# Optimization experiments

Measured on AMD Instinct MI355X. Metric: run time of the kernel, lower is better.

Reference implementation:

```python
import jax, jax.numpy as jnp
import numpy as np

EPS = 1e-12  # matches torch.nn.functional.normalize default eps


def _l2norm(x, axis=-1):
    # F.normalize: x / max(||x||, eps)
    n = jnp.sqrt(jnp.sum(x * x, axis=axis, keepdims=True))
    return x / jnp.maximum(n, EPS)


def setup_inputs() -> dict:
    key = jax.random.key(0)
    k1, k2, k3 = jax.random.split(key, 3)
    batch, n_mels, time_steps = 32, 80, 4000
    num_codebooks, codebook_size, d = 2, 1024, 64
    mel = jax.random.normal(k1, (batch, n_mels, time_steps), dtype=jnp.float32)
    proj = jax.random.normal(k2, (num_codebooks, n_mels, d), dtype=jnp.float32)
    codebooks = jax.random.normal(k3, (num_codebooks, codebook_size, d), dtype=jnp.float32)
    return {"mel": mel, "proj": proj, "codebooks": codebooks}


def reference(mel, proj, codebooks):
    # mel: [b, n, t] -> [b, t, n]
    mel_t = jnp.transpose(mel, (0, 2, 1))
    # project for all codebooks at once: [c, b, t, d]
    p = jnp.einsum('btn,cnd->cbtd', mel_t, proj)
    p = _l2norm(p, axis=-1)
    cb = _l2norm(codebooks, axis=-1)  # [c, k, d]
    # cosine similarity: [c, b, t, k]
    sim = jnp.einsum('cbtd,ckd->cbtk', p, cb)
    codes = jnp.argmax(sim, axis=-1)  # [c, b, t]
    return codes
```

## Files before the change

kernel.cpp:

```cpp
#include <hip/hip_runtime.h>
#include <hip/hip_bf16.h>
#include <math.h>
#include <stdint.h>


#define B      32
#define NMELS  80
#define TSTEPS 4000
#define NCB    2
#define KCB    1024
#define DDIM   64
#define TPB    256
#define TM     64
#define KT     64
#define NKT    (KCB / KT)
#define PPAD   66

typedef short bf16x8 __attribute__((ext_vector_type(8)));
typedef float f32x4  __attribute__((ext_vector_type(4)));

#define WS_CB_OFF   8192
#define WS_NEEDED   (8192 + NCB*KCB*DDIM*2)

static __device__ __forceinline__ uint32_t bits(float f) {
    return __builtin_bit_cast(uint32_t, f);
}
static __device__ __forceinline__ float fbits(uint32_t u) {
    return __builtin_bit_cast(float, u);
}
static __device__ __forceinline__ uint32_t rne16(uint32_t u) {
    return (u + 0x7FFFu + ((u >> 16) & 1u)) >> 16;
}

__global__ __launch_bounds__(TPB) void rpq_prep(const float* __restrict__ cb,
                                                float* __restrict__ ws)
{
    const int idx = blockIdx.x * TPB + threadIdx.x;
    if (idx >= NCB * KCB) return;

    const float4* row = (const float4*)(cb + (size_t)idx * DDIM);
    float4 v[16];
    float ss = 0.f;
    #pragma unroll
    for (int i = 0; i < 16; ++i) {
        v[i] = row[i];
        ss += v[i].x*v[i].x + v[i].y*v[i].y + v[i].z*v[i].z + v[i].w*v[i].w;
    }
    const float inv = 1.0f / fmaxf(sqrtf(ss), 1e-12f);
    ws[idx] = inv;

    uint32_t dw[32];
    #pragma unroll
    for (int i = 0; i < 16; ++i) {
        dw[2*i]   = rne16(bits(v[i].x * inv)) | (rne16(bits(v[i].y * inv)) << 16);
        dw[2*i+1] = rne16(bits(v[i].z * inv)) | (rne16(bits(v[i].w * inv)) << 16);
    }
    uint4* dst = (uint4*)((char*)ws + WS_CB_OFF + (size_t)idx * 128);
    #pragma unroll
    for (int i = 0; i < 8; ++i)
        dst[i] = make_uint4(dw[4*i], dw[4*i+1], dw[4*i+2], dw[4*i+3]);
}

__global__ __launch_bounds__(TPB, 4) void rpq_main(
    const float* __restrict__ mel,
    const float* __restrict__ proj,
    const float* __restrict__ cb,
    const float* __restrict__ ws,
    int* __restrict__ out)
{
    const int tid  = threadIdx.x;
    const int b    = blockIdx.y;
    const int c    = blockIdx.z;
    const int t0   = blockIdx.x * TM;

    const int l    = tid & 63;
    const int wid  = tid >> 6;
    const int lrow = l & 15;
    const int lgrp = l >> 4;

    __shared__ union __align__(16) {
        float projS[NMELS * DDIM];
        struct {
            union {
                char cbuf[2][KT * 128];
                struct {
                    uint32_t cand[TM][17][2];
                    float    scv[TM][8];
                    int      sck[TM][8];
                } m;
            } a;
            float PL[TM * PPAD];
        } p2;
    } U;

    const char*  wscb   = (const char*)ws + WS_CB_OFF + (size_t)c * (KCB * 128);
    const float* invn_g = ws + (size_t)c * KCB;

    {
        const float4* src = (const float4*)(proj + (size_t)c * NMELS * DDIM);
        float4* dst = (float4*)U.projS;
        for (int i = tid; i < NMELS * DDIM / 4; i += TPB) dst[i] = src[i];
    }
    __syncthreads();

    const int srow = tid >> 2;
    const int sq   = tid & 3;
    uint4 g0, g1;
    {
        const uint4* gp = (const uint4*)(wscb + (size_t)srow * 128 + sq * 32);
        g0 = gp[0]; g1 = gp[1];
    }

    {
        const int tq = tid & 15;
        const int dg = tid >> 4;
        const int tbase  = t0 + tq * 4;
        const int tb_c   = (tbase <= TSTEPS - 4) ? tbase : (TSTEPS - 4);
        const float* mp  = mel + (size_t)b * NMELS * TSTEPS + tb_c;

        float Pa[4][4];
        #pragma unroll
        for (int i = 0; i < 4; ++i)
            #pragma unroll
            for (int j = 0; j < 4; ++j) Pa[i][j] = 0.f;

        for (int n = 0; n < NMELS; ++n) {
            const float4 m4 = *(const float4*)(mp + (size_t)n * TSTEPS);
            const float4 w  = *(const float4*)&U.projS[n * DDIM + dg * 4];
            Pa[0][0] = fmaf(m4.x, w.x, Pa[0][0]); Pa[0][1] = fmaf(m4.x, w.y, Pa[0][1]);
            Pa[0][2] = fmaf(m4.x, w.z, Pa[0][2]); Pa[0][3] = fmaf(m4.x, w.w, Pa[0][3]);
            Pa[1][0] = fmaf(m4.y, w.x, Pa[1][0]); Pa[1][1] = fmaf(m4.y, w.y, Pa[1][1]);
            Pa[1][2] = fmaf(m4.y, w.z, Pa[1][2]); Pa[1][3] = fmaf(m4.y, w.w, Pa[1][3]);
            Pa[2][0] = fmaf(m4.z, w.x, Pa[2][0]); Pa[2][1] = fmaf(m4.z, w.y, Pa[2][1]);
            Pa[2][2] = fmaf(m4.z, w.z, Pa[2][2]); Pa[2][3] = fmaf(m4.z, w.w, Pa[2][3]);
            Pa[3][0] = fmaf(m4.w, w.x, Pa[3][0]); Pa[3][1] = fmaf(m4.w, w.y, Pa[3][1]);
            Pa[3][2] = fmaf(m4.w, w.z, Pa[3][2]); Pa[3][3] = fmaf(m4.w, w.w, Pa[3][3]);
        }
        __syncthreads();

        #pragma unroll
        for (int i = 0; i < 4; ++i)
            *(float4*)&U.p2.PL[(tq * 4 + i) * PPAD + dg * 4] =
                make_float4(Pa[i][0], Pa[i][1], Pa[i][2], Pa[i][3]);
    }

    {
        const int xw = (srow & 7) << 4;
        char* base = &U.p2.a.cbuf[0][srow * 128];
        *(uint4*)(base + ((sq * 32)      ^ xw)) = g0;
        *(uint4*)(base + ((sq * 32 + 16) ^ xw)) = g1;
    }
    __syncthreads();

    bf16x8 A0, A1;
    {
        const float* pr = &U.p2.PL[((wid << 4) + lrow) * PPAD];
        #pragma unroll
        for (int i = 0; i < 8; ++i) {
            A0[i] = (short)rne16(bits(pr[lgrp * 8 + i]));
            A1[i] = (short)rne16(bits(pr[32 + lgrp * 8 + i]));
        }
    }

    float m1[4], m2[4];
    #pragma unroll
    for (int r = 0; r < 4; ++r) { m1[r] = -INFINITY; m2[r] = -INFINITY; }
    uint32_t idxv = (uint32_t)(1023 - lrow);

    const int xr  = (lrow & 7) << 4;
    const int bo0 = (lgrp * 16) ^ xr;
    const int bo1 = (64 + lgrp * 16) ^ xr;

    for (int kt = 0; kt < NKT; ++kt) {
        const int cur = kt & 1;
        if (kt + 1 < NKT) {
            const uint4* gp = (const uint4*)(wscb + (size_t)(kt + 1) * (KT * 128)
                                             + (size_t)srow * 128 + sq * 32);
            g0 = gp[0]; g1 = gp[1];
        }
        const char* buf = U.p2.a.cbuf[cur];
        #pragma unroll
        for (int s = 0; s < 4; ++s) {
            const char* rowp = buf + (s * 16 + lrow) * 128;
            bf16x8 B0 = *(const bf16x8*)(rowp + bo0);
            bf16x8 B1 = *(const bf16x8*)(rowp + bo1);
            f32x4 acc = {0.f, 0.f, 0.f, 0.f};
            acc = __builtin_amdgcn_mfma_f32_16x16x32_bf16(A0, B0, acc, 0, 0, 0);
            acc = __builtin_amdgcn_mfma_f32_16x16x32_bf16(A1, B1, acc, 0, 0, 0);
            #pragma unroll
            for (int r = 0; r < 4; ++r) {
                const float pf = fbits((bits(acc[r]) & 0xFFFFFC00u) | idxv);
                m2[r] = __builtin_amdgcn_fmed3f(pf, m1[r], m2[r]);
                m1[r] = fmaxf(pf, m1[r]);
            }
            idxv -= 16u;
        }
        if (kt + 1 < NKT) {
            const int xw = (srow & 7) << 4;
            char* base = &U.p2.a.cbuf[cur ^ 1][srow * 128];
            *(uint4*)(base + ((sq * 32)      ^ xw)) = g0;
            *(uint4*)(base + ((sq * 32 + 16) ^ xw)) = g1;
        }
        __syncthreads();
    }

    #pragma unroll
    for (int r = 0; r < 4; ++r) {
        const int trow = (wid << 4) + (lgrp << 2) + r;
        U.p2.a.m.cand[trow][lrow][0] = bits(m1[r]);
        U.p2.a.m.cand[trow][lrow][1] = bits(m2[r]);
    }
    __syncthreads();

    {
        const int t = tid & 63;
        const int j = wid;
        float c1 = -INFINITY, c2 = -INFINITY, c3 = -INFINITY, c4 = -INFINITY;
        float c5 = -INFINITY, c6 = -INFINITY, c7 = -INFINITY, c8 = -INFINITY;
        for (int i = 0; i < 16; ++i) {
            #pragma unroll
            for (int jj = 0; jj < 2; ++jj) {
                const float p = fbits(U.p2.a.m.cand[t][i][jj]);
                c8 = fmaxf(fminf(p, c7), c8);
                c7 = fmaxf(fminf(p, c6), c7);
                c6 = fmaxf(fminf(p, c5), c6);
                c5 = fmaxf(fminf(p, c4), c5);
                c4 = fmaxf(fminf(p, c3), c4);
                c3 = fmaxf(fminf(p, c2), c3);
                c2 = fmaxf(fminf(p, c1), c2);
                c1 = fmaxf(p, c1);
            }
        }
        const float sel0 = (j == 0) ? c1 : (j == 1) ? c3 : (j == 2) ? c5 : c7;
        const float sel1 = (j == 0) ? c2 : (j == 1) ? c4 : (j == 2) ? c6 : c8;
        const float* pr  = &U.p2.PL[t * PPAD];
        const float* cbc = cb + (size_t)c * KCB * DDIM;
        #pragma unroll
        for (int e = 0; e < 2; ++e) {
            const float sel = e ? sel1 : sel0;
            const int kj = 1023 - (int)(bits(sel) & 0x3FFu);
            const float* cbr = cbc + (size_t)kj * DDIM;
            float a0 = 0.f, a1 = 0.f, a2 = 0.f, a3 = 0.f;
            #pragma unroll
            for (int i = 0; i < 16; ++i) {
                float4 pv = *(const float4*)(pr + i * 4);
                float4 cv = *(const float4*)(cbr + i * 4);
                a0 = fmaf(pv.x, cv.x, a0); a1 = fmaf(pv.y, cv.y, a1);
                a2 = fmaf(pv.z, cv.z, a2); a3 = fmaf(pv.w, cv.w, a3);
            }
            U.p2.a.m.scv[t][2*j + e] = ((a0 + a1) + (a2 + a3)) * invn_g[kj];
            U.p2.a.m.sck[t][2*j + e] = kj;
        }
    }
    __syncthreads();

    if (tid < TM) {
        const int tg = t0 + tid;
        if (tg < TSTEPS) {
            float best = U.p2.a.m.scv[tid][0];
            int   bk   = U.p2.a.m.sck[tid][0];
            #pragma unroll
            for (int s2 = 1; s2 < 8; ++s2) {
                const float v = U.p2.a.m.scv[tid][s2];
                const int  kk = U.p2.a.m.sck[tid][s2];
                if (v > best || (v == best && kk < bk)) { best = v; bk = kk; }
            }
            out[((size_t)c * B + b) * TSTEPS + tg] = bk;
        }
    }
}

__global__ __launch_bounds__(TPB, 2) void rpq_fallback(
    const float* __restrict__ mel, const float* __restrict__ proj,
    const float* __restrict__ cb, int* __restrict__ out)
{
    const int tid = threadIdx.x;
    const int b = blockIdx.y, c = blockIdx.z;
    const int t0 = blockIdx.x * (TPB * 2) + tid;
    const int t1 = t0 + TPB;
    const int tc0 = (t0 < TSTEPS) ? t0 : (TSTEPS - 1);
    const int tc1 = (t1 < TSTEPS) ? t1 : (TSTEPS - 1);

    __shared__ union { float projS[NMELS*DDIM]; float cbS[2][64*DDIM]; } sh;
    __shared__ float invn[KCB];
    const float* cbc = cb + (size_t)c * KCB * DDIM;
    {
        const float4* src = (const float4*)(proj + (size_t)c * NMELS * DDIM);
        float4* dst = (float4*)sh.projS;
        for (int i = tid; i < NMELS*DDIM/4; i += TPB) dst[i] = src[i];
    }
    for (int j = 0; j < KCB/TPB; ++j) {
        const int k = j*TPB + tid;
        const float4* r = (const float4*)(cbc + (size_t)k * DDIM);
        float s = 0.f;
        #pragma unroll
        for (int i = 0; i < DDIM/4; ++i) {
            float4 v = r[i]; s += v.x*v.x + v.y*v.y + v.z*v.z + v.w*v.w;
        }
        invn[k] = 1.0f / fmaxf(sqrtf(s), 1e-12f);
    }
    float4 r0, r1, r2, r3;
    { const float4* g = (const float4*)cbc;
      r0 = g[tid]; r1 = g[tid+256]; r2 = g[tid+512]; r3 = g[tid+768]; }
    __syncthreads();
    float P0[DDIM], P1[DDIM];
    #pragma unroll
    for (int d = 0; d < DDIM; ++d) { P0[d] = 0.f; P1[d] = 0.f; }
    const float* mp = mel + (size_t)b * NMELS * TSTEPS;
    for (int n = 0; n < NMELS; ++n) {
        const float m0 = mp[(size_t)n*TSTEPS + tc0];
        const float m1_ = mp[(size_t)n*TSTEPS + tc1];
        const float4* ps = (const float4*)(sh.projS + n*DDIM);
        #pragma unroll
        for (int i = 0; i < DDIM/4; ++i) {
            float4 v = ps[i];
            P0[4*i+0]=fmaf(m0,v.x,P0[4*i+0]); P0[4*i+1]=fmaf(m0,v.y,P0[4*i+1]);
            P0[4*i+2]=fmaf(m0,v.z,P0[4*i+2]); P0[4*i+3]=fmaf(m0,v.w,P0[4*i+3]);
            P1[4*i+0]=fmaf(m1_,v.x,P1[4*i+0]); P1[4*i+1]=fmaf(m1_,v.y,P1[4*i+1]);
            P1[4*i+2]=fmaf(m1_,v.z,P1[4*i+2]); P1[4*i+3]=fmaf(m1_,v.w,P1[4*i+3]);
        }
    }
    __syncthreads();
    { float4* dst = (float4*)sh.cbS[0];
      dst[tid]=r0; dst[tid+256]=r1; dst[tid+512]=r2; dst[tid+768]=r3; }
    { const float4* g = (const float4*)(cbc + (size_t)64*DDIM);
      r0=g[tid]; r1=g[tid+256]; r2=g[tid+512]; r3=g[tid+768]; }
    __syncthreads();
    float best0 = -INFINITY, best1 = -INFINITY; int bi0 = 0, bi1 = 0;
    for (int kt = 0; kt < KCB/64; ++kt) {
        const int cur = kt & 1;
        const float* base = sh.cbS[cur];
        const int kbase = kt * 64;
        #pragma unroll 2
        for (int kk = 0; kk < 64; ++kk) {
            const float4* row = (const float4*)(base + kk*DDIM);
            float a0=0,a1=0,a2=0,a3=0,b0=0,b1=0,b2=0,b3=0;
            #pragma unroll
            for (int i = 0; i < DDIM/4; ++i) {
                float4 v = row[i];
                a0=fmaf(P0[4*i+0],v.x,a0); a1=fmaf(P0[4*i+1],v.y,a1);
                a2=fmaf(P0[4*i+2],v.z,a2); a3=fmaf(P0[4*i+3],v.w,a3);
                b0=fmaf(P1[4*i+0],v.x,b0); b1=fmaf(P1[4*i+1],v.y,b1);
                b2=fmaf(P1[4*i+2],v.z,b2); b3=fmaf(P1[4*i+3],v.w,b3);
            }
            const int k = kbase + kk;
            const float w = invn[k];
            const float s0 = ((a0+a1)+(a2+a3))*w;
            const float s1 = ((b0+b1)+(b2+b3))*w;
            if (s0 > best0) { best0 = s0; bi0 = k; }
            if (s1 > best1) { best1 = s1; bi1 = k; }
        }
        if (kt + 1 < KCB/64) {
            float4* dst = (float4*)sh.cbS[cur ^ 1];
            dst[tid]=r0; dst[tid+256]=r1; dst[tid+512]=r2; dst[tid+768]=r3;
            if (kt + 2 < KCB/64) {
                const float4* g = (const float4*)(cbc + (size_t)(kt+2)*64*DDIM);
                r0=g[tid]; r1=g[tid+256]; r2=g[tid+512]; r3=g[tid+768];
            }
        }
        __syncthreads();
    }
    const size_t ob = ((size_t)c * B + b) * TSTEPS;
    if (t0 < TSTEPS) out[ob + t0] = bi0;
    if (t1 < TSTEPS) out[ob + t1] = bi1;
}

extern "C" void kernel_launch(void* const* d_in, const int* in_sizes, int n_in,
                              void* d_out, int out_size, void* d_ws, size_t ws_size,
                              hipStream_t stream) {
    const float* mel  = (const float*)d_in[0];
    const float* proj = (const float*)d_in[1];
    const float* cb   = (const float*)d_in[2];
    int* out = (int*)d_out;

    if (ws_size >= (size_t)WS_NEEDED) {
        float* ws = (float*)d_ws;
        rpq_prep<<<dim3((NCB*KCB + TPB - 1)/TPB), dim3(TPB), 0, stream>>>(cb, ws);
        dim3 grid((TSTEPS + TM - 1) / TM, B, NCB);
        rpq_main<<<grid, dim3(TPB), 0, stream>>>(mel, proj, cb, ws, out);
    } else {
        dim3 grid((TSTEPS + TPB*2 - 1) / (TPB*2), B, NCB);
        rpq_fallback<<<grid, dim3(TPB), 0, stream>>>(mel, proj, cb, out);
    }
}
```

Before: 167.7 us.

## Halve codebook tile to 32 rows and raise occupancy to five blocks

The codebook staging tile shrinks from 64 to 32 rows, so each thread loads one uint4 per tile instead of two and the double buffer takes half the LDS. Launch bounds go from 4 to 5 blocks per SM, and the candidate buffer is transposed to [16][TM][2] so the merge loop reads each pair with one 8-byte load. The score arrays are moved out of the union. The aim is more waves in flight to hide load and barrier latency, at the cost of twice as many loop iterations and barriers and tighter register limits.

```diff
diff --git a/kernel.cpp b/kernel.cpp
--- a/kernel.cpp
+++ b/kernel.cpp
@@ -12,7 +12,7 @@
 #define DDIM   64
 #define TPB    256
 #define TM     64
-#define KT     64
+#define KT     32
 #define NKT    (KCB / KT)
 #define PPAD   66
 
@@ -61,7 +61,7 @@
         dst[i] = make_uint4(dw[4*i], dw[4*i+1], dw[4*i+2], dw[4*i+3]);
 }
 
-__global__ __launch_bounds__(TPB, 4) void rpq_main(
+__global__ __launch_bounds__(TPB, 5) void rpq_main(
     const float* __restrict__ mel,
     const float* __restrict__ proj,
     const float* __restrict__ cb,
@@ -82,14 +82,12 @@
         float projS[NMELS * DDIM];
         struct {
             union {
-                char cbuf[2][KT * 128];
-                struct {
-                    uint32_t cand[TM][17][2];
-                    float    scv[TM][8];
-                    int      sck[TM][8];
-                } m;
+                char     cbuf[2][KT * 128];
+                uint32_t candT[16][TM][2];
             } a;
             float PL[TM * PPAD];
+            float scv[TM][9];
+            int   sck[TM][9];
         } p2;
     } U;
 
@@ -103,13 +101,10 @@
     }
     __syncthreads();
 
-    const int srow = tid >> 2;
-    const int sq   = tid & 3;
-    uint4 g0, g1;
-    {
-        const uint4* gp = (const uint4*)(wscb + (size_t)srow * 128 + sq * 32);
-        g0 = gp[0]; g1 = gp[1];
-    }
+    const int srow = tid >> 3;
+    const int sq   = tid & 7;
+    uint4 g0;
+    g0 = *(const uint4*)(wscb + (size_t)tid * 16);
 
     {
         const int tq = tid & 15;
@@ -146,9 +141,7 @@
 
     {
         const int xw = (srow & 7) << 4;
-        char* base = &U.p2.a.cbuf[0][srow * 128];
-        *(uint4*)(base + ((sq * 32)      ^ xw)) = g0;
-        *(uint4*)(base + ((sq * 32 + 16) ^ xw)) = g1;
+        *(uint4*)(&U.p2.a.cbuf[0][srow * 128] + ((sq * 16) ^ xw)) = g0;
     }
     __syncthreads();
 
@@ -174,13 +167,12 @@
     for (int kt = 0; kt < NKT; ++kt) {
         const int cur = kt & 1;
         if (kt + 1 < NKT) {
-            const uint4* gp = (const uint4*)(wscb + (size_t)(kt + 1) * (KT * 128)
-                                             + (size_t)srow * 128 + sq * 32);
-            g0 = gp[0]; g1 = gp[1];
+            g0 = *(const uint4*)(wscb + (size_t)(kt + 1) * (KT * 128)
+                                 + (size_t)tid * 16);
         }
         const char* buf = U.p2.a.cbuf[cur];
         #pragma unroll
-        for (int s = 0; s < 4; ++s) {
+        for (int s = 0; s < 2; ++s) {
             const char* rowp = buf + (s * 16 + lrow) * 128;
             bf16x8 B0 = *(const bf16x8*)(rowp + bo0);
             bf16x8 B1 = *(const bf16x8*)(rowp + bo1);
@@ -189,7 +181,8 @@
             acc = __builtin_amdgcn_mfma_f32_16x16x32_bf16(A1, B1, acc, 0, 0, 0);
             #pragma unroll
             for (int r = 0; r < 4; ++r) {
-                const float pf = fbits((bits(acc[r]) & 0xFFFFFC00u) | idxv);
+                const float pf = fbits((bits(acc[r]) & 0xFFFFFC00u)
+                                     | (idxv & 0x3FFu));
                 m2[r] = __builtin_amdgcn_fmed3f(pf, m1[r], m2[r]);
                 m1[r] = fmaxf(pf, m1[r]);
             }
@@ -197,9 +190,7 @@
         }
         if (kt + 1 < NKT) {
             const int xw = (srow & 7) << 4;
-            char* base = &U.p2.a.cbuf[cur ^ 1][srow * 128];
-            *(uint4*)(base + ((sq * 32)      ^ xw)) = g0;
-            *(uint4*)(base + ((sq * 32 + 16) ^ xw)) = g1;
+            *(uint4*)(&U.p2.a.cbuf[cur ^ 1][srow * 128] + ((sq * 16) ^ xw)) = g0;
         }
         __syncthreads();
     }
@@ -207,8 +198,8 @@
     #pragma unroll
     for (int r = 0; r < 4; ++r) {
         const int trow = (wid << 4) + (lgrp << 2) + r;
-        U.p2.a.m.cand[trow][lrow][0] = bits(m1[r]);
-        U.p2.a.m.cand[trow][lrow][1] = bits(m2[r]);
+        U.p2.a.candT[lrow][trow][0] = bits(m1[r]);
+        U.p2.a.candT[lrow][trow][1] = bits(m2[r]);
     }
     __syncthreads();
 
@@ -218,9 +209,10 @@
         float c1 = -INFINITY, c2 = -INFINITY, c3 = -INFINITY, c4 = -INFINITY;
         float c5 = -INFINITY, c6 = -INFINITY, c7 = -INFINITY, c8 = -INFINITY;
         for (int i = 0; i < 16; ++i) {
+            const uint2 pv2 = *(const uint2*)&U.p2.a.candT[i][t][0];
             #pragma unroll
             for (int jj = 0; jj < 2; ++jj) {
-                const float p = fbits(U.p2.a.m.cand[t][i][jj]);
+                const float p = fbits(jj ? pv2.y : pv2.x);
                 c8 = fmaxf(fminf(p, c7), c8);
                 c7 = fmaxf(fminf(p, c6), c7);
                 c6 = fmaxf(fminf(p, c5), c6);
@@ -248,8 +240,8 @@
                 a0 = fmaf(pv.x, cv.x, a0); a1 = fmaf(pv.y, cv.y, a1);
                 a2 = fmaf(pv.z, cv.z, a2); a3 = fmaf(pv.w, cv.w, a3);
             }
-            U.p2.a.m.scv[t][2*j + e] = ((a0 + a1) + (a2 + a3)) * invn_g[kj];
-            U.p2.a.m.sck[t][2*j + e] = kj;
+            U.p2.scv[t][2*j + e] = ((a0 + a1) + (a2 + a3)) * invn_g[kj];
+            U.p2.sck[t][2*j + e] = kj;
         }
     }
     __syncthreads();
@@ -257,12 +249,12 @@
     if (tid < TM) {
         const int tg = t0 + tid;
         if (tg < TSTEPS) {
-            float best = U.p2.a.m.scv[tid][0];
-            int   bk   = U.p2.a.m.sck[tid][0];
+            float best = U.p2.scv[tid][0];
+            int   bk   = U.p2.sck[tid][0];
             #pragma unroll
             for (int s2 = 1; s2 < 8; ++s2) {
-                const float v = U.p2.a.m.scv[tid][s2];
-                const int  kk = U.p2.a.m.sck[tid][s2];
+                const float v = U.p2.scv[tid][s2];
+                const int  kk = U.p2.sck[tid][s2];
                 if (v > best || (v == best && kk < bk)) { best = v; bk = kk; }
             }
             out[((size_t)c * B + b) * TSTEPS + tg] = bk;
```

Result: slower. 193.1 us (+15.1%).
